# Optimization experiments

Hardware: AMD Instinct MI355X
Metric: run time of the kernel (lower is better)

## Reference

```python
import jax, jax.numpy as jnp
import numpy as np

EPS = 1e-3
LOG2PI = float(np.log(2.0 * np.pi))

# dims
B, Z, Y, T, D = 32768, 256, 32, 64, 4  # batch, z_dim, y_dim, n_types, type_dim


def setup_inputs() -> dict:
    key = jax.random.key(0)
    ks = jax.random.split(key, 8)
    z = jax.random.normal(ks[0], (B, Z), dtype=jnp.float32)
    batch_x = jax.random.normal(ks[1], (B, T, D), dtype=jnp.float32)
    miss_list = jax.random.randint(ks[2], (B, T), 0, 2, dtype=jnp.int32)  # 1=observed, 0=missing
    data_mean = jax.random.normal(ks[3], (T, D), dtype=jnp.float32)
    data_var = jax.random.uniform(ks[4], (T, D), dtype=jnp.float32, minval=0.5, maxval=1.5)
    # weights init N(0, 0.005) as in the torch module; biases zero
    Wy = jax.random.normal(ks[5], (T * Y, Z), dtype=jnp.float32) * 0.005
    by = jnp.zeros((T * Y,), dtype=jnp.float32)
    Wm = jax.random.normal(ks[6], (T, D, Y), dtype=jnp.float32) * 0.005
    bm = jnp.zeros((T, D), dtype=jnp.float32)
    Wv = jax.random.normal(ks[7], (T, D, Y), dtype=jnp.float32) * 0.005
    bv = jnp.zeros((T, D), dtype=jnp.float32)
    return {"z": z, "batch_x": batch_x, "miss_list": miss_list,
            "data_mean": data_mean, "data_var": data_var,
            "Wy": Wy, "by": by, "Wm": Wm, "bm": bm, "Wv": Wv, "bv": bv}


def reference(z, batch_x, miss_list, data_mean, data_var, Wy, by, Wm, bm, Wv, bv):
    # y_layer: z -> [B, T*Y], grouped into per-type gamma slices [B, T, Y]
    y = z @ Wy.T + by
    gamma = y.reshape(y.shape[0], T, Y)

    mask = miss_list.astype(gamma.dtype)            # [B, T], 1=observed
    m3 = mask[:, :, None]                           # [B, T, 1]

    # per-type tiny linears (dynamic_partition + Linear + dynamic_stitch).
    # Numerically: same linear on all rows; missing rows are under no_grad,
    # realized here as stop_gradient on the missing partition.
    lin_m = jnp.einsum('bty,tdy->btd', gamma, Wm) + bm   # [B, T, D]
    lin_v = jnp.einsum('bty,tdy->btd', gamma, Wv) + bv
    est_mean = m3 * lin_m + (1.0 - m3) * jax.lax.stop_gradient(lin_m)
    est_var_raw = m3 * lin_v + (1.0 - m3) * jax.lax.stop_gradient(lin_v)

    # loglik_real: softplus variance, denormalize with data mean/var
    dvar = jnp.clip(data_var, EPS)
    est_var = jnp.clip(jax.nn.softplus(est_var_raw), EPS, 1e20)
    mean_x = jnp.sqrt(dvar) * est_mean + data_mean       # [B, T, D]
    var_x = dvar * est_var                               # [B, T, D]

    log_p = -0.5 * jnp.sum((batch_x - mean_x) ** 2 / var_x + jnp.log(var_x) + LOG2PI, axis=-1)  # [B, T]
    log_p_x = log_p * mask
    log_p_x_missing = log_p * (1.0 - mask)
    return (log_p_x, log_p_x_missing, mean_x, var_x)
```

## Files before the change

kernel.cpp:

```cpp
#include <hip/hip_runtime.h>


#define Bsz   32768
#define Tsz   64
#define Dsz   4
#define Ysz   32
#define Zsz   256
#define Nsz   512
#define BTtot (Bsz * Tsz)
#define EPS_  1e-3f
#define LOG2PI_ 1.8378770664093453f

#define BM       64
#define NT       512
#define ASTRIDE  264
#define LSTRIDE2 72

typedef __attribute__((ext_vector_type(4))) float  f32x4;
typedef __attribute__((ext_vector_type(8))) short  short8;
typedef __attribute__((ext_vector_type(2))) unsigned int uint2v;

static __device__ __forceinline__ unsigned short f2bf(float f) {
    unsigned int u = __float_as_uint(f);
    return (unsigned short)((u + 0x7fffu + ((u >> 16) & 1u)) >> 16);
}
static __device__ __forceinline__ float bf2f(unsigned short h) {
    return __uint_as_float(((unsigned int)h) << 16);
}
static __device__ __forceinline__ unsigned int cvt_pk_bf16(float a, float b) {
    unsigned int r;
    asm("v_cvt_pk_bf16_f32 %0, %1, %2" : "=v"(r) : "v"(a), "v"(b));
    return r;
}

__global__ __launch_bounds__(256)
void hidec_prep(const float* __restrict__ Wy, const float* __restrict__ by,
                const float* __restrict__ Wm, const float* __restrict__ bm,
                const float* __restrict__ Wv, const float* __restrict__ bv,
                unsigned short* __restrict__ weff, float* __restrict__ beff) {
    __shared__ float Ml[8][Ysz];
    __shared__ float byl[Ysz];
    const int t   = blockIdx.x;
    const int tid = threadIdx.x;
    {
        int j = tid >> 5, y = tid & 31;
        const float* src = (j < 4) ? Wm : Wv;
        Ml[j][y] = src[(t * Dsz + (j & 3)) * Ysz + y];
    }
    if (tid < Ysz) byl[tid] = by[t * Ysz + tid];
    __syncthreads();

    const int k = tid;
    const int kk = k >> 5, q = (k >> 3) & 3, je = k & 7;
    float wy[Ysz];
#pragma unroll
    for (int y = 0; y < Ysz; ++y)
        wy[y] = Wy[(size_t)(t * Ysz + y) * Zsz + k];
#pragma unroll
    for (int j = 0; j < 8; ++j) {
        float acc = 0.f;
#pragma unroll
        for (int y = 0; y < Ysz; ++y) acc = fmaf(Ml[j][y], wy[y], acc);
        int n   = t * 8 + j;
        int tau = n >> 4, c = n & 15;
        weff[((((tau * 8 + kk) * 4 + q) * 16 + c) * 8) + je] = f2bf(acc);
    }
    if (tid < 8) {
        int d = tid & 3;
        float s = ((tid < 4) ? bm : bv)[t * Dsz + d];
        for (int y = 0; y < Ysz; ++y) s = fmaf(byl[y], Ml[tid][y], s);
        beff[t * 8 + tid] = s;
    }
}

__global__ __launch_bounds__(NT, 4)
void hidec_main(const float* __restrict__ z, const float* __restrict__ bx,
                const int* __restrict__ miss, const float* __restrict__ dmean,
                const float* __restrict__ dvarp, const unsigned short* __restrict__ weff,
                const float* __restrict__ beff, float* __restrict__ out) {
    __shared__ unsigned short buf[BM * ASTRIDE + 8 * 32 * LSTRIDE2];
    __shared__ float4 sqA[Tsz], dmA[Tsz], dcA[Tsz];
    __shared__ float  sldv[Tsz];
    __shared__ float  beffL[Nsz];

    const int tid  = threadIdx.x;
    const long row0 = (long)blockIdx.x * BM;

    if (tid < Tsz) {
        float4 dv4 = *(const float4*)(dvarp + tid * 4);
        float4 dm4 = *(const float4*)(dmean + tid * 4);
        float d0 = fmaxf(dv4.x, EPS_), d1 = fmaxf(dv4.y, EPS_);
        float d2 = fmaxf(dv4.z, EPS_), d3 = fmaxf(dv4.w, EPS_);
        sqA[tid] = (float4){sqrtf(d0), sqrtf(d1), sqrtf(d2), sqrtf(d3)};
        dmA[tid] = dm4;
        dcA[tid] = (float4){d0, d1, d2, d3};
        sldv[tid] = __logf(d0) + __logf(d1) + __logf(d2) + __logf(d3);
    }
    beffL[tid] = beff[tid];

    unsigned short* a_lds = buf;
#pragma unroll
    for (int i = 0; i < 8; ++i) {
        int idx4 = tid + i * NT;
        int r  = idx4 >> 6;
        int c4 = idx4 & 63;
        float4 v = *(const float4*)(z + (row0 + r) * Zsz + c4 * 4);
        uint2v p;
        p.x = cvt_pk_bf16(v.x, v.y);
        p.y = cvt_pk_bf16(v.z, v.w);
        *(uint2v*)&a_lds[r * ASTRIDE + c4 * 4] = p;
    }
    __syncthreads();

    const int lane = tid & 63;
    const int w    = tid >> 6;
    const int c    = lane & 15;
    const int q    = lane >> 4;

    f32x4 acc[16];
#pragma unroll
    for (int i = 0; i < 16; ++i) acc[i] = (f32x4){0.f, 0.f, 0.f, 0.f};

    const unsigned short* wp = weff + ((size_t)(w * 4) * 8) * 512 + lane * 8;

#pragma unroll
    for (int kk = 0; kk < 8; ++kk) {
        short8 b0 = *(const short8*)(wp + kk * 512 + 0 * 4096);
        short8 b1 = *(const short8*)(wp + kk * 512 + 1 * 4096);
        short8 b2 = *(const short8*)(wp + kk * 512 + 2 * 4096);
        short8 b3 = *(const short8*)(wp + kk * 512 + 3 * 4096);
        short8 a0 = *(const short8*)&a_lds[(0 * 16 + c) * ASTRIDE + kk * 32 + q * 8];
        short8 a1 = *(const short8*)&a_lds[(1 * 16 + c) * ASTRIDE + kk * 32 + q * 8];
        short8 a2 = *(const short8*)&a_lds[(2 * 16 + c) * ASTRIDE + kk * 32 + q * 8];
        short8 a3 = *(const short8*)&a_lds[(3 * 16 + c) * ASTRIDE + kk * 32 + q * 8];
        acc[0]  = __builtin_amdgcn_mfma_f32_16x16x32_bf16(a0, b0, acc[0],  0, 0, 0);
        acc[1]  = __builtin_amdgcn_mfma_f32_16x16x32_bf16(a1, b0, acc[1],  0, 0, 0);
        acc[2]  = __builtin_amdgcn_mfma_f32_16x16x32_bf16(a2, b0, acc[2],  0, 0, 0);
        acc[3]  = __builtin_amdgcn_mfma_f32_16x16x32_bf16(a3, b0, acc[3],  0, 0, 0);
        acc[4]  = __builtin_amdgcn_mfma_f32_16x16x32_bf16(a0, b1, acc[4],  0, 0, 0);
        acc[5]  = __builtin_amdgcn_mfma_f32_16x16x32_bf16(a1, b1, acc[5],  0, 0, 0);
        acc[6]  = __builtin_amdgcn_mfma_f32_16x16x32_bf16(a2, b1, acc[6],  0, 0, 0);
        acc[7]  = __builtin_amdgcn_mfma_f32_16x16x32_bf16(a3, b1, acc[7],  0, 0, 0);
        acc[8]  = __builtin_amdgcn_mfma_f32_16x16x32_bf16(a0, b2, acc[8],  0, 0, 0);
        acc[9]  = __builtin_amdgcn_mfma_f32_16x16x32_bf16(a1, b2, acc[9],  0, 0, 0);
        acc[10] = __builtin_amdgcn_mfma_f32_16x16x32_bf16(a2, b2, acc[10], 0, 0, 0);
        acc[11] = __builtin_amdgcn_mfma_f32_16x16x32_bf16(a3, b2, acc[11], 0, 0, 0);
        acc[12] = __builtin_amdgcn_mfma_f32_16x16x32_bf16(a0, b3, acc[12], 0, 0, 0);
        acc[13] = __builtin_amdgcn_mfma_f32_16x16x32_bf16(a1, b3, acc[13], 0, 0, 0);
        acc[14] = __builtin_amdgcn_mfma_f32_16x16x32_bf16(a2, b3, acc[14], 0, 0, 0);
        acc[15] = __builtin_amdgcn_mfma_f32_16x16x32_bf16(a3, b3, acc[15], 0, 0, 0);
    }

    unsigned short* lw = buf + BM * ASTRIDE + w * (32 * LSTRIDE2);

    float bb[4];
#pragma unroll
    for (int ti = 0; ti < 4; ++ti) bb[ti] = beffL[w * 64 + ti * 16 + c];

#pragma unroll
    for (int h = 0; h < 2; ++h) {
#pragma unroll
        for (int ti = 0; ti < 4; ++ti) {
            int cb = ti * 16 + c;
#pragma unroll
            for (int rh = 0; rh < 2; ++rh) {
                const f32x4 a = acc[ti * 4 + (2 * h + rh)];
                unsigned int p01 = cvt_pk_bf16(a[0] + bb[ti], a[1] + bb[ti]);
                unsigned int p23 = cvt_pk_bf16(a[2] + bb[ti], a[3] + bb[ti]);
                int rbase = rh * 16 + q * 4;
                lw[(rbase + 0) * LSTRIDE2 + cb] = (unsigned short)(p01 & 0xffffu);
                lw[(rbase + 1) * LSTRIDE2 + cb] = (unsigned short)(p01 >> 16);
                lw[(rbase + 2) * LSTRIDE2 + cb] = (unsigned short)(p23 & 0xffffu);
                lw[(rbase + 3) * LSTRIDE2 + cb] = (unsigned short)(p23 >> 16);
            }
        }
        asm volatile("s_waitcnt lgkmcnt(0)" ::: "memory");

#pragma unroll
        for (int p = 0; p < 4; ++p) {
            int rloc = p * 8 + (lane >> 3);
            int tl   = lane & 7;
            int t    = w * 8 + tl;
            long bt  = (row0 + h * 32 + rloc) * Tsz + t;

            short8 l8 = *(const short8*)&lw[rloc * LSTRIDE2 + tl * 8];
            float lm[4], lv[4];
#pragma unroll
            for (int d = 0; d < 4; ++d) {
                lm[d] = bf2f((unsigned short)l8[d]);
                lv[d] = bf2f((unsigned short)l8[4 + d]);
            }

            float4 x4  = *(const float4*)(bx + bt * 4);
            float mk   = (float)miss[bt];
            float4 sq4 = sqA[t];
            float4 dm4 = dmA[t];
            float4 dc4 = dcA[t];
            float xa[4]  = {x4.x,  x4.y,  x4.z,  x4.w};
            float sqa[4] = {sq4.x, sq4.y, sq4.z, sq4.w};
            float dma[4] = {dm4.x, dm4.y, dm4.z, dm4.w};
            float dca[4] = {dc4.x, dc4.y, dc4.z, dc4.w};

            float mean_o[4], var_o[4];
            float s = sldv[t];
            float evp = 1.f;
#pragma unroll
            for (int d = 0; d < 4; ++d) {
                float mean = fmaf(sqa[d], lm[d], dma[d]);
                float v    = lv[d];
                float sp   = fmaxf(v, 0.f) + __logf(1.f + __expf(-fabsf(v)));
                float ev   = fminf(fmaxf(sp, EPS_), 1e20f);
                float var  = dca[d] * ev;
                float diff = xa[d] - mean;
                s = fmaf(diff * diff, __builtin_amdgcn_rcpf(var), s);
                evp *= ev;
                mean_o[d] = mean;
                var_o[d]  = var;
            }
            s += __logf(evp);
            float logp = -0.5f * (s + 4.f * LOG2PI_);

            float lx = logp * mk;
            out[bt]         = lx;
            out[BTtot + bt] = logp - lx;

            *(float4*)(out + 2L * BTtot + bt * 4) =
                (float4){mean_o[0], mean_o[1], mean_o[2], mean_o[3]};
            *(float4*)(out + 6L * BTtot + bt * 4) =
                (float4){var_o[0], var_o[1], var_o[2], var_o[3]};
        }
    }
}

extern "C" void kernel_launch(void* const* d_in, const int* in_sizes, int n_in,
                              void* d_out, int out_size, void* d_ws, size_t ws_size,
                              hipStream_t stream) {
    const float* z     = (const float*)d_in[0];
    const float* bx    = (const float*)d_in[1];
    const int*   miss  = (const int*)d_in[2];
    const float* dmean = (const float*)d_in[3];
    const float* dvar  = (const float*)d_in[4];
    const float* Wy    = (const float*)d_in[5];
    const float* by    = (const float*)d_in[6];
    const float* Wm    = (const float*)d_in[7];
    const float* bm    = (const float*)d_in[8];
    const float* Wv    = (const float*)d_in[9];
    const float* bv    = (const float*)d_in[10];
    float* out = (float*)d_out;

    unsigned short* weff = (unsigned short*)d_ws;
    float* beff = (float*)((char*)d_ws + (size_t)Nsz * Zsz * 2);

    hidec_prep<<<Tsz, Zsz, 0, stream>>>(Wy, by, Wm, bm, Wv, bv, weff, beff);
    hidec_main<<<Bsz / BM, NT, 0, stream>>>(z, bx, miss, dmean, dvar, weff, beff, out);
}
```

Measured before the change: 179.7 us.

## Halve row tile to 32, raise occupancy, compute per-type constants in registers

Shrinks the per-block row tile from 64 to 32, halving the MFMA accumulator count and LDS footprint, and raises the launch-bounds occupancy hint from 4 to 8 blocks. It also drops the shared-memory tables for data variance, mean and bias: each thread now computes its type's constants in registers and reads the bias straight from global memory. The aim is more concurrent waves to hide the latency of the memory-bound epilogue. The cost is twice as many blocks, each reloading the weight fragments with less reuse per load, plus tighter per-thread register limits.

Measured after the change: 191.1 us. +6.3%, slower.

```diff
diff --git a/kernel.cpp b/kernel.cpp
--- a/kernel.cpp
+++ b/kernel.cpp
@@ -11,7 +11,7 @@
 #define EPS_  1e-3f
 #define LOG2PI_ 1.8378770664093453f
 
-#define BM       64
+#define BM       32
 #define NT       512
 #define ASTRIDE  264
 #define LSTRIDE2 72
@@ -73,42 +73,27 @@
     }
 }
 
-__global__ __launch_bounds__(NT, 4)
+__global__ __launch_bounds__(NT, 8)
 void hidec_main(const float* __restrict__ z, const float* __restrict__ bx,
                 const int* __restrict__ miss, const float* __restrict__ dmean,
                 const float* __restrict__ dvarp, const unsigned short* __restrict__ weff,
                 const float* __restrict__ beff, float* __restrict__ out) {
-    __shared__ unsigned short buf[BM * ASTRIDE + 8 * 32 * LSTRIDE2];
-    __shared__ float4 sqA[Tsz], dmA[Tsz], dcA[Tsz];
-    __shared__ float  sldv[Tsz];
-    __shared__ float  beffL[Nsz];
+    __shared__ unsigned short buf[BM * ASTRIDE + 8 * 16 * LSTRIDE2];
 
     const int tid  = threadIdx.x;
     const long row0 = (long)blockIdx.x * BM;
 
-    if (tid < Tsz) {
-        float4 dv4 = *(const float4*)(dvarp + tid * 4);
-        float4 dm4 = *(const float4*)(dmean + tid * 4);
-        float d0 = fmaxf(dv4.x, EPS_), d1 = fmaxf(dv4.y, EPS_);
-        float d2 = fmaxf(dv4.z, EPS_), d3 = fmaxf(dv4.w, EPS_);
-        sqA[tid] = (float4){sqrtf(d0), sqrtf(d1), sqrtf(d2), sqrtf(d3)};
-        dmA[tid] = dm4;
-        dcA[tid] = (float4){d0, d1, d2, d3};
-        sldv[tid] = __logf(d0) + __logf(d1) + __logf(d2) + __logf(d3);
-    }
-    beffL[tid] = beff[tid];
-
     unsigned short* a_lds = buf;
 #pragma unroll
-    for (int i = 0; i < 8; ++i) {
+    for (int i = 0; i < 4; ++i) {
         int idx4 = tid + i * NT;
         int r  = idx4 >> 6;
         int c4 = idx4 & 63;
         float4 v = *(const float4*)(z + (row0 + r) * Zsz + c4 * 4);
-        uint2v p;
-        p.x = cvt_pk_bf16(v.x, v.y);
-        p.y = cvt_pk_bf16(v.z, v.w);
-        *(uint2v*)&a_lds[r * ASTRIDE + c4 * 4] = p;
+        uint2v pk;
+        pk.x = cvt_pk_bf16(v.x, v.y);
+        pk.y = cvt_pk_bf16(v.z, v.w);
+        *(uint2v*)&a_lds[r * ASTRIDE + c4 * 4] = pk;
     }
     __syncthreads();
 
@@ -117,9 +102,9 @@
     const int c    = lane & 15;
     const int q    = lane >> 4;
 
-    f32x4 acc[16];
-#pragma unroll
-    for (int i = 0; i < 16; ++i) acc[i] = (f32x4){0.f, 0.f, 0.f, 0.f};
+    f32x4 acc[8];
+#pragma unroll
+    for (int i = 0; i < 8; ++i) acc[i] = (f32x4){0.f, 0.f, 0.f, 0.f};
 
     const unsigned short* wp = weff + ((size_t)(w * 4) * 8) * 512 + lane * 8;
 
@@ -131,57 +116,52 @@
         short8 b3 = *(const short8*)(wp + kk * 512 + 3 * 4096);
         short8 a0 = *(const short8*)&a_lds[(0 * 16 + c) * ASTRIDE + kk * 32 + q * 8];
         short8 a1 = *(const short8*)&a_lds[(1 * 16 + c) * ASTRIDE + kk * 32 + q * 8];
-        short8 a2 = *(const short8*)&a_lds[(2 * 16 + c) * ASTRIDE + kk * 32 + q * 8];
-        short8 a3 = *(const short8*)&a_lds[(3 * 16 + c) * ASTRIDE + kk * 32 + q * 8];
-        acc[0]  = __builtin_amdgcn_mfma_f32_16x16x32_bf16(a0, b0, acc[0],  0, 0, 0);
-        acc[1]  = __builtin_amdgcn_mfma_f32_16x16x32_bf16(a1, b0, acc[1],  0, 0, 0);
-        acc[2]  = __builtin_amdgcn_mfma_f32_16x16x32_bf16(a2, b0, acc[2],  0, 0, 0);
-        acc[3]  = __builtin_amdgcn_mfma_f32_16x16x32_bf16(a3, b0, acc[3],  0, 0, 0);
-        acc[4]  = __builtin_amdgcn_mfma_f32_16x16x32_bf16(a0, b1, acc[4],  0, 0, 0);
-        acc[5]  = __builtin_amdgcn_mfma_f32_16x16x32_bf16(a1, b1, acc[5],  0, 0, 0);
-        acc[6]  = __builtin_amdgcn_mfma_f32_16x16x32_bf16(a2, b1, acc[6],  0, 0, 0);
-        acc[7]  = __builtin_amdgcn_mfma_f32_16x16x32_bf16(a3, b1, acc[7],  0, 0, 0);
-        acc[8]  = __builtin_amdgcn_mfma_f32_16x16x32_bf16(a0, b2, acc[8],  0, 0, 0);
-        acc[9]  = __builtin_amdgcn_mfma_f32_16x16x32_bf16(a1, b2, acc[9],  0, 0, 0);
-        acc[10] = __builtin_amdgcn_mfma_f32_16x16x32_bf16(a2, b2, acc[10], 0, 0, 0);
-        acc[11] = __builtin_amdgcn_mfma_f32_16x16x32_bf16(a3, b2, acc[11], 0, 0, 0);
-        acc[12] = __builtin_amdgcn_mfma_f32_16x16x32_bf16(a0, b3, acc[12], 0, 0, 0);
-        acc[13] = __builtin_amdgcn_mfma_f32_16x16x32_bf16(a1, b3, acc[13], 0, 0, 0);
-        acc[14] = __builtin_amdgcn_mfma_f32_16x16x32_bf16(a2, b3, acc[14], 0, 0, 0);
-        acc[15] = __builtin_amdgcn_mfma_f32_16x16x32_bf16(a3, b3, acc[15], 0, 0, 0);
-    }
-
-    unsigned short* lw = buf + BM * ASTRIDE + w * (32 * LSTRIDE2);
+        acc[0] = __builtin_amdgcn_mfma_f32_16x16x32_bf16(a0, b0, acc[0], 0, 0, 0);
+        acc[1] = __builtin_amdgcn_mfma_f32_16x16x32_bf16(a1, b0, acc[1], 0, 0, 0);
+        acc[2] = __builtin_amdgcn_mfma_f32_16x16x32_bf16(a0, b1, acc[2], 0, 0, 0);
+        acc[3] = __builtin_amdgcn_mfma_f32_16x16x32_bf16(a1, b1, acc[3], 0, 0, 0);
+        acc[4] = __builtin_amdgcn_mfma_f32_16x16x32_bf16(a0, b2, acc[4], 0, 0, 0);
+        acc[5] = __builtin_amdgcn_mfma_f32_16x16x32_bf16(a1, b2, acc[5], 0, 0, 0);
+        acc[6] = __builtin_amdgcn_mfma_f32_16x16x32_bf16(a0, b3, acc[6], 0, 0, 0);
+        acc[7] = __builtin_amdgcn_mfma_f32_16x16x32_bf16(a1, b3, acc[7], 0, 0, 0);
+    }
+
+    unsigned short* lw = buf + BM * ASTRIDE + w * (16 * LSTRIDE2);
+
+    const int tl = lane & 7;
+    const int t  = w * 8 + tl;
+    float4 dv4 = *(const float4*)(dvarp + t * 4);
+    float4 dm4 = *(const float4*)(dmean + t * 4);
+    float dca[4] = {fmaxf(dv4.x, EPS_), fmaxf(dv4.y, EPS_),
+                    fmaxf(dv4.z, EPS_), fmaxf(dv4.w, EPS_)};
+    float sqa[4] = {sqrtf(dca[0]), sqrtf(dca[1]), sqrtf(dca[2]), sqrtf(dca[3])};
+    float dma[4] = {dm4.x, dm4.y, dm4.z, dm4.w};
+    float sldv = __logf(dca[0]) + __logf(dca[1]) + __logf(dca[2]) + __logf(dca[3]);
 
     float bb[4];
 #pragma unroll
-    for (int ti = 0; ti < 4; ++ti) bb[ti] = beffL[w * 64 + ti * 16 + c];
+    for (int ti = 0; ti < 4; ++ti) bb[ti] = beff[w * 64 + ti * 16 + c];
 
 #pragma unroll
     for (int h = 0; h < 2; ++h) {
 #pragma unroll
         for (int ti = 0; ti < 4; ++ti) {
             int cb = ti * 16 + c;
-#pragma unroll
-            for (int rh = 0; rh < 2; ++rh) {
-                const f32x4 a = acc[ti * 4 + (2 * h + rh)];
-                unsigned int p01 = cvt_pk_bf16(a[0] + bb[ti], a[1] + bb[ti]);
-                unsigned int p23 = cvt_pk_bf16(a[2] + bb[ti], a[3] + bb[ti]);
-                int rbase = rh * 16 + q * 4;
-                lw[(rbase + 0) * LSTRIDE2 + cb] = (unsigned short)(p01 & 0xffffu);
-                lw[(rbase + 1) * LSTRIDE2 + cb] = (unsigned short)(p01 >> 16);
-                lw[(rbase + 2) * LSTRIDE2 + cb] = (unsigned short)(p23 & 0xffffu);
-                lw[(rbase + 3) * LSTRIDE2 + cb] = (unsigned short)(p23 >> 16);
-            }
+            const f32x4 a = acc[ti * 2 + h];
+            unsigned int p01 = cvt_pk_bf16(a[0] + bb[ti], a[1] + bb[ti]);
+            unsigned int p23 = cvt_pk_bf16(a[2] + bb[ti], a[3] + bb[ti]);
+            int rbase = q * 4;
+            lw[(rbase + 0) * LSTRIDE2 + cb] = (unsigned short)(p01 & 0xffffu);
+            lw[(rbase + 1) * LSTRIDE2 + cb] = (unsigned short)(p01 >> 16);
+            lw[(rbase + 2) * LSTRIDE2 + cb] = (unsigned short)(p23 & 0xffffu);
+            lw[(rbase + 3) * LSTRIDE2 + cb] = (unsigned short)(p23 >> 16);
         }
         asm volatile("s_waitcnt lgkmcnt(0)" ::: "memory");
 
 #pragma unroll
-        for (int p = 0; p < 4; ++p) {
-            int rloc = p * 8 + (lane >> 3);
-            int tl   = lane & 7;
-            int t    = w * 8 + tl;
-            long bt  = (row0 + h * 32 + rloc) * Tsz + t;
+        for (int pp = 0; pp < 2; ++pp) {
+            int rloc = pp * 8 + (lane >> 3);
+            long bt  = (row0 + h * 16 + rloc) * Tsz + t;
 
             short8 l8 = *(const short8*)&lw[rloc * LSTRIDE2 + tl * 8];
             float lm[4], lv[4];
@@ -193,16 +173,10 @@
 
             float4 x4  = *(const float4*)(bx + bt * 4);
             float mk   = (float)miss[bt];
-            float4 sq4 = sqA[t];
-            float4 dm4 = dmA[t];
-            float4 dc4 = dcA[t];
             float xa[4]  = {x4.x,  x4.y,  x4.z,  x4.w};
-            float sqa[4] = {sq4.x, sq4.y, sq4.z, sq4.w};
-            float dma[4] = {dm4.x, dm4.y, dm4.z, dm4.w};
-            float dca[4] = {dc4.x, dc4.y, dc4.z, dc4.w};
 
             float mean_o[4], var_o[4];
-            float s = sldv[t];
+            float s = sldv;
             float evp = 1.f;
 #pragma unroll
             for (int d = 0; d < 4; ++d) {
```
